# Kernel tuning notes

Measured on AMD Instinct MI355X. Metric: run time of the kernel, lower is better.

Reference implementation:

```python
import jax, jax.numpy as jnp
import numpy as np

COORD_W, WIDTH_W, VALID_W = 5.0, 1.0, 1.0  # module init defaults
COST_COORD_W, COST_WIDTH_W = 5.0, 1.0      # hardcoded in compute_cost_matrix


def _hungarian(cost):
    """Pure-numpy linear_sum_assignment (Jonker-Volgenant style, e-maxx variant).
    cost: [R, C] float. Returns (row_ind, col_ind) matching scipy semantics
    (min(R, C) pairs minimizing total cost)."""
    cost = np.asarray(cost, dtype=np.float64)
    transposed = cost.shape[0] > cost.shape[1]
    C = cost.T if transposed else cost
    n, m = C.shape  # n <= m
    u = np.zeros(n + 1)
    v = np.zeros(m + 1)
    p = np.zeros(m + 1, dtype=np.int64)   # p[j] = 1-indexed row assigned to col j
    way = np.zeros(m + 1, dtype=np.int64)
    for i in range(1, n + 1):
        p[0] = i
        j0 = 0
        minv = np.full(m + 1, np.inf)
        used = np.zeros(m + 1, dtype=bool)
        while True:
            used[j0] = True
            i0 = p[j0]
            jf = np.nonzero(~used[1:])[0] + 1  # free columns (1-indexed)
            cur = C[i0 - 1, jf - 1] - u[i0] - v[jf]
            upd = cur < minv[jf]
            minv[jf] = np.where(upd, cur, minv[jf])
            way[jf[upd]] = j0
            j1 = jf[np.argmin(minv[jf])]
            delta = minv[j1]
            u[p[used]] += delta
            v[used] -= delta
            minv[jf] -= delta
            j0 = j1
            if p[j0] == 0:
                break
        while j0:
            j1 = way[j0]
            p[j0] = p[j1]
            j0 = j1
    col4row = np.zeros(n, dtype=np.int64)
    for j in range(1, m + 1):
        if p[j] > 0:
            col4row[p[j] - 1] = j - 1
    rows = np.arange(n, dtype=np.int64)
    return (col4row, rows) if transposed else (rows, col4row)


def _compute_matching(pred_strokes, targets):
    """Per-batch Hungarian matching on the (detached) cost matrix.
    Returns padded pred idx P [B,S], gt idx G [B,S], match mask M [B,S], num_gt N [B]."""
    ps = np.asarray(pred_strokes)
    tg = np.asarray(targets)
    B, S, _ = ps.shape
    P = np.zeros((B, S), dtype=np.int64)
    G = np.zeros((B, S), dtype=np.int64)
    M = np.zeros((B, S), dtype=np.float32)
    N = np.zeros((B,), dtype=np.float32)
    for b in range(B):
        valid = np.nonzero(tg[b, :, 10] > 0.5)[0]
        ng = len(valid)
        N[b] = ng
        if ng == 0:
            continue
        gt = tg[b, valid, :10]                      # [ng, 10]
        d = np.abs(ps[b, :, None, :] - gt[None])    # [S, ng, 10]
        cost = COST_COORD_W * d[..., :8].sum(-1) + COST_WIDTH_W * d[..., 8:10].sum(-1)
        pi, gi = _hungarian(cost)
        P[b, :ng] = pi
        G[b, :ng] = valid[gi]
        M[b, :ng] = 1.0
    return P, G, M, N


def _loss(pred_strokes, pred_validity, targets, P, G, M, N):
    gt_strokes = targets[..., :10]
    gt_val = targets[..., 10:11]
    mp = jnp.take_along_axis(pred_strokes, P[..., None], axis=1)  # [B,S,10]
    mg = jnp.take_along_axis(gt_strokes, G[..., None], axis=1)    # [B,S,10]
    ad = jnp.abs(mp - mg) * M[..., None]
    ng = jnp.maximum(N, 1.0)
    coord = ad[..., :8].sum(axis=(1, 2)) / (ng * 8.0)             # per-batch L1 mean
    width = ad[..., 8:10].sum(axis=(1, 2)) / (ng * 2.0)
    # BCE with torch-style log clamp at -100
    logp = jnp.clip(jnp.log(pred_validity), -100.0)
    log1p = jnp.clip(jnp.log(1.0 - pred_validity), -100.0)
    bce = (-(gt_val * logp + (1.0 - gt_val) * log1p)).mean(axis=(1, 2))
    loss_b = jnp.where(N > 0, COORD_W * coord + WIDTH_W * width + VALID_W * bce, bce)
    return loss_b.mean()


def setup_inputs() -> dict:
    key = jax.random.key(0)
    k1, k2, k3 = jax.random.split(key, 3)
    B, S = 256, 64
    return {
        "pred_strokes": jax.random.uniform(k1, (B, S, 10), dtype=jnp.float32),
        "pred_validity": jax.random.uniform(k2, (B, S, 1), dtype=jnp.float32),
        "targets": jax.random.uniform(k3, (B, S, 11), dtype=jnp.float32),
    }


def reference(pred_strokes, pred_validity, targets):
    P, G, M, N = _compute_matching(pred_strokes, targets)
    return _loss(pred_strokes, pred_validity, targets,
                 jnp.asarray(P), jnp.asarray(G), jnp.asarray(M), jnp.asarray(N))
```

## Files before the change

### kernel.cpp

```cpp
#include <hip/hip_runtime.h>
#include <math.h>


#define SS 64
#define LDS_FENCE() asm volatile("s_waitcnt lgkmcnt(0)" ::: "memory")

__device__ __forceinline__ int rlane_i(int x, int lane) {
    return __builtin_amdgcn_readlane(x, lane);
}

__global__ __launch_bounds__(64) void detr_match_loss_kernel(
    const float* __restrict__ pred_strokes,
    const float* __restrict__ pred_validity,
    const float* __restrict__ targets,
    double* __restrict__ loss_ws)
{
    const int b = blockIdx.x;
    const int t = threadIdx.x;
    const float* ps = pred_strokes  + (size_t)b * SS * 10;
    const float* pv = pred_validity + (size_t)b * SS;
    const float* tg = targets      + (size_t)b * SS * 11;

    __shared__ float  Cs[SS * SS];
    __shared__ float  tgs[SS * 11];
    __shared__ double u_lds[SS + 1];
    __shared__ int    vidx[SS];
    __shared__ int    col4row[SS];

#pragma unroll
    for (int k = 0; k < 11; ++k) tgs[k * SS + t] = tg[k * SS + t];
    LDS_FENCE();

    const float gv    = tgs[t * 11 + 10];
    const bool  valid = gv > 0.5f;
    const unsigned long long vmask = __ballot(valid);
    const int ng = __popcll(vmask);
    if (valid) {
        const int rank = __popcll(vmask & ((1ull << t) - 1ull));
        vidx[rank] = t;
    }
    LDS_FENCE();

    double bterm;
    {
        const float pvv = pv[t];
        const float lp  = fmaxf(logf(pvv), -100.0f);
        const float l1p = fmaxf(logf(1.0f - pvv), -100.0f);
        bterm = -((double)gv * (double)lp + (double)(1.0f - gv) * (double)l1p);
    }

    double csum = 0.0, wsum = 0.0;

    if (ng > 0) {
        float pr[10];
#pragma unroll
        for (int k = 0; k < 10; ++k) pr[k] = ps[t * 10 + k];

        for (int i = 0; i < ng; ++i) {
            const float* g = &tgs[vidx[i] * 11];
            float d[10];
#pragma unroll
            for (int k = 0; k < 10; ++k) d[k] = fabsf(pr[k] - g[k]);
            const float cs = ((d[0] + d[1]) + (d[2] + d[3]))
                           + ((d[4] + d[5]) + (d[6] + d[7]));
            const float wd = d[8] + d[9];
            float c;
            {
#pragma clang fp contract(off)
                c = 5.0f * cs + wd;
            }
            Cs[i * SS + t] = c;
        }
        LDS_FENCE();

        double v_j = 0.0;
        int    p_j = 0;

        for (int i = 1; i <= ng; ++i) {
            double minv_j = __builtin_inf();
            int    way_j  = 0;
            bool   used_j = false;
            double usum   = 0.0;
            double u0     = 0.0;
            int    j0     = 0;
            float  Cval   = Cs[(i - 1) * SS + t];

            for (;;) {
                if (t + 1 == j0) used_j = true;
                const double cur = ((double)Cval - u0) - v_j;
                if (!used_j && cur < minv_j) { minv_j = cur; way_j = j0; }

                const double mvl = used_j ? __builtin_inf() : minv_j;
                double m = mvl;
#pragma unroll
                for (int off = 1; off < 64; off <<= 1)
                    m = fmin(m, __shfl_xor(m, off, 64));
                const unsigned long long bal = __ballot(mvl == m);
                const int j1 = __builtin_amdgcn_readfirstlane(
                                   __ffsll((unsigned long long)bal));
                const int i1 = rlane_i(p_j, j1 - 1);

                double u_next = 0.0; float C_next = 0.0f;
                if (i1 != 0) {
                    u_next = u_lds[i1];
                    C_next = Cs[(i1 - 1) * SS + t];
                }

                usum += m;
                if (used_j) {
                    v_j -= m;
                    u_lds[p_j] += m;
                } else {
                    minv_j -= m;
                }

                j0 = j1;
                if (i1 == 0) break;
                u0 = u_next; Cval = C_next;
            }

            int jj = j0;
            while (jj != 0) {
                const int jp   = rlane_i(way_j, jj - 1);
                const int pnew = (jp == 0) ? i : rlane_i(p_j, jp - 1);
                if (t == jj - 1) p_j = pnew;
                jj = jp;
            }
            if (t == 0) u_lds[i] = usum;
            LDS_FENCE();
        }

        if (p_j > 0) col4row[p_j - 1] = t;
        LDS_FENCE();

        if (t < ng) {
            const float* g  = &tgs[vidx[t] * 11];
            const float* mp = ps + col4row[t] * 10;
#pragma unroll
            for (int k = 0; k < 8; ++k) csum += (double)fabsf(mp[k] - g[k]);
            wsum = (double)fabsf(mp[8] - g[8]) + (double)fabsf(mp[9] - g[9]);
        }
    }

    double s0 = csum, s1 = wsum, s2 = bterm;
#pragma unroll
    for (int off = 1; off < 64; off <<= 1) {
        s0 += __shfl_xor(s0, off, 64);
        s1 += __shfl_xor(s1, off, 64);
        s2 += __shfl_xor(s2, off, 64);
    }
    if (t == 0) {
        const double bce = s2 / 64.0;
        const double loss = (ng > 0)
            ? 5.0 * (s0 / ((double)ng * 8.0)) + (s1 / ((double)ng * 2.0)) + bce
            : bce;
        loss_ws[b] = loss;
    }
}

__global__ __launch_bounds__(256) void detr_reduce_kernel(
    const double* __restrict__ ws, float* __restrict__ out, int B)
{
    const int t = threadIdx.x;
    double x = 0.0;
    for (int idx = t; idx < B; idx += 256) x += ws[idx];
    for (int off = 1; off < 64; off <<= 1) x += __shfl_xor(x, off, 64);
    __shared__ double part[4];
    if ((t & 63) == 0) part[t >> 6] = x;
    __syncthreads();
    if (t == 0) {
        double s = part[0] + part[1] + part[2] + part[3];
        out[0] = (float)(s / (double)B);
    }
}

extern "C" void kernel_launch(void* const* d_in, const int* in_sizes, int n_in,
                              void* d_out, int out_size, void* d_ws, size_t ws_size,
                              hipStream_t stream) {
    const float* ps = (const float*)d_in[0];
    const float* pv = (const float*)d_in[1];
    const float* tg = (const float*)d_in[2];
    float* out = (float*)d_out;
    double* ws = (double*)d_ws;
    const int B = in_sizes[0] / (SS * 10);

    detr_match_loss_kernel<<<B, SS, 0, stream>>>(ps, pv, tg, ws);
    detr_reduce_kernel<<<1, 256, 0, stream>>>(ws, out, B);
}
```

Baseline: 100.1 us.

## Replace shuffle-based double min with DPP u32 key reduction and register-resident duals

The wave argmin over the double minv now reduces only the high 32 bits with DPP row shifts, falling back to a second pass on the low word only when several lanes tie. The row potentials u move from LDS into per-lane registers and are fetched with readlane, which removes the LDS writes and fences in the inner augmenting loop. The next row's cost value is prefetched. The aim is a shorter per-iteration latency chain in the serial Hungarian loop, at the cost of extra ballots and a second reduction when high words tie. The high-word-as-unsigned ordering assumes minv values are nonnegative, which holds because reduced costs stay nonnegative.

```diff
diff --git a/kernel.cpp b/kernel.cpp
--- a/kernel.cpp
+++ b/kernel.cpp
@@ -7,6 +7,26 @@
 
 __device__ __forceinline__ int rlane_i(int x, int lane) {
     return __builtin_amdgcn_readlane(x, lane);
+}
+__device__ __forceinline__ double rlane_d(double x, int lane) {
+    return __hiloint2double(rlane_i(__double2hiint(x), lane),
+                            rlane_i(__double2loint(x), lane));
+}
+
+template<int CTRL>
+__device__ __forceinline__ unsigned dpp_shift_ff(unsigned x) {
+    return (unsigned)__builtin_amdgcn_update_dpp(
+        (int)0xFFFFFFFFu, (int)x, CTRL, 0xF, 0xF, false);
+}
+__device__ __forceinline__ unsigned wave_min_u32_to63(unsigned x) {
+    unsigned y;
+    y = dpp_shift_ff<0x111>(x); x = x < y ? x : y;
+    y = dpp_shift_ff<0x112>(x); x = x < y ? x : y;
+    y = dpp_shift_ff<0x114>(x); x = x < y ? x : y;
+    y = dpp_shift_ff<0x118>(x); x = x < y ? x : y;
+    y = dpp_shift_ff<0x142>(x); x = x < y ? x : y;
+    y = dpp_shift_ff<0x143>(x); x = x < y ? x : y;
+    return x;
 }
 
 __global__ __launch_bounds__(64) void detr_match_loss_kernel(
@@ -23,7 +43,6 @@
 
     __shared__ float  Cs[SS * SS];
     __shared__ float  tgs[SS * 11];
-    __shared__ double u_lds[SS + 1];
     __shared__ int    vidx[SS];
     __shared__ int    col4row[SS];
 
@@ -71,53 +90,62 @@
             }
             Cs[i * SS + t] = c;
         }
-        LDS_FENCE();
-
-        double v_j = 0.0;
-        int    p_j = 0;
+
+        double v_j   = 0.0;
+        double u_reg = 0.0;
+        int    p_j   = 0;
+        float  Chead = Cs[t];
 
         for (int i = 1; i <= ng; ++i) {
-            double minv_j = __builtin_inf();
-            int    way_j  = 0;
-            bool   used_j = false;
-            double usum   = 0.0;
-            double u0     = 0.0;
-            int    j0     = 0;
-            float  Cval   = Cs[(i - 1) * SS + t];
+            double minv_j   = __builtin_inf();
+            int    way_j    = 0;
+            bool   used_j   = false;
+            bool   row_used = (t == i - 1);
+            double u0       = 0.0;
+            int    j0       = 0;
+            float  Cval     = Chead;
 
             for (;;) {
-                if (t + 1 == j0) used_j = true;
+                used_j = used_j || (t + 1 == j0);
                 const double cur = ((double)Cval - u0) - v_j;
                 if (!used_j && cur < minv_j) { minv_j = cur; way_j = j0; }
 
-                const double mvl = used_j ? __builtin_inf() : minv_j;
-                double m = mvl;
-#pragma unroll
-                for (int off = 1; off < 64; off <<= 1)
-                    m = fmin(m, __shfl_xor(m, off, 64));
-                const unsigned long long bal = __ballot(mvl == m);
-                const int j1 = __builtin_amdgcn_readfirstlane(
-                                   __ffsll((unsigned long long)bal));
-                const int i1 = rlane_i(p_j, j1 - 1);
-
-                double u_next = 0.0; float C_next = 0.0f;
-                if (i1 != 0) {
-                    u_next = u_lds[i1];
-                    C_next = Cs[(i1 - 1) * SS + t];
+                const unsigned key = used_j ? 0x7FF00000u
+                                            : (unsigned)__double2hiint(minv_j);
+                const unsigned kr    = wave_min_u32_to63(key);
+                const unsigned hstar = (unsigned)rlane_i((int)kr, 63);
+                unsigned long long bal = __ballot(key == hstar);
+                int j1 = __ffsll(bal);
+                int i1 = rlane_i(p_j, j1 - 1);
+
+                float C_next = 0.0f;
+                if (i1 != 0) C_next = Cs[(i1 - 1) * SS + t];
+
+                if (__popcll(bal) > 1) {
+                    const unsigned lo = (key == hstar)
+                        ? (unsigned)__double2loint(minv_j) : 0xFFFFFFFFu;
+                    const unsigned lr    = wave_min_u32_to63(lo);
+                    const unsigned lstar = (unsigned)rlane_i((int)lr, 63);
+                    bal = __ballot(key == hstar && lo == lstar);
+                    j1  = __ffsll(bal);
+                    i1  = rlane_i(p_j, j1 - 1);
+                    if (i1 != 0) C_next = Cs[(i1 - 1) * SS + t];
                 }
 
-                usum += m;
-                if (used_j) {
-                    v_j -= m;
-                    u_lds[p_j] += m;
-                } else {
-                    minv_j -= m;
-                }
+                const double delta  = rlane_d(minv_j, j1 - 1);
+                const double u_next = (i1 != 0) ? rlane_d(u_reg, i1 - 1) : 0.0;
+
+                if (row_used) u_reg += delta;
+                if (used_j)   v_j   -= delta;
+                else          minv_j -= delta;
+                row_used = row_used || (t == i1 - 1);
 
                 j0 = j1;
                 if (i1 == 0) break;
                 u0 = u_next; Cval = C_next;
             }
+
+            Chead = (i < ng) ? Cs[i * SS + t] : 0.0f;
 
             int jj = j0;
             while (jj != 0) {
@@ -126,8 +154,6 @@
                 if (t == jj - 1) p_j = pnew;
                 jj = jp;
             }
-            if (t == 0) u_lds[i] = usum;
-            LDS_FENCE();
         }
 
         if (p_j > 0) col4row[p_j - 1] = t;
```

After: 86.14 us. -14.0%, faster.
